# Optimization experiments

Measured on AMD Instinct MI355X. Metric: run time of the kernel, lower is better.

## Reference

```python
import jax, jax.numpy as jnp
import numpy as np

DIM = 1024
HEADS = 16

def setup_inputs() -> dict:
    key = jax.random.key(0)
    k1, k2, k3, k4 = jax.random.split(key, 4)
    x = jax.random.normal(k1, (2, 2048, DIM), dtype=jnp.float32)
    ln_gamma = jnp.ones((DIM,), dtype=jnp.float32)
    ln_beta = jnp.zeros((DIM,), dtype=jnp.float32)
    # torch Linear weight is [out, in]; store transposed [in, out] for x @ W
    W_qkv = jax.random.normal(k2, (DIM, 3 * DIM), dtype=jnp.float32) * (DIM ** -0.5)
    W_out = jax.random.normal(k3, (DIM, DIM), dtype=jnp.float32) * (DIM ** -0.5)
    b_out = jax.random.normal(k4, (DIM,), dtype=jnp.float32) * 0.02
    return {"x": x, "ln_gamma": ln_gamma, "ln_beta": ln_beta,
            "W_qkv": W_qkv, "W_out": W_out, "b_out": b_out}

def reference(x, ln_gamma, ln_beta, W_qkv, W_out, b_out):
    B, N, C = x.shape
    H = HEADS
    Dh = C // H
    scale = Dh ** -0.5
    # LayerNorm (eps=1e-5, torch default)
    mu = jnp.mean(x, axis=-1, keepdims=True)
    var = jnp.var(x, axis=-1, keepdims=True)
    xn = (x - mu) / jnp.sqrt(var + 1e-5) * ln_gamma + ln_beta
    # QKV projection: [B,N,3C] -> [3,B,H,N,Dh]
    qkv = (xn @ W_qkv).reshape(B, N, 3, H, Dh).transpose(2, 0, 3, 1, 4)
    q, k, v = qkv[0], qkv[1], qkv[2]
    attn = jnp.einsum('bhnd,bhmd->bhnm', q, k) * scale  # [B,H,N,N]
    attn = jax.nn.softmax(attn, axis=-1)
    out = jnp.einsum('bhnm,bhmd->bhnd', attn, v)  # [B,H,N,Dh]
    out = out.transpose(0, 2, 1, 3).reshape(B, N, C)
    return out @ W_out + b_out
```

## Files before the change

### kernel.cpp

```cpp
#include <hip/hip_runtime.h>
#include <hip/hip_bf16.h>

#define DIM 1024
#define HEADS 16
#define DH 64
#define SEQ 2048
#define BATCH 2
#define ROWS (BATCH*SEQ)
#define C3 (3*DIM)

typedef __attribute__((ext_vector_type(8))) short s16x8;
typedef __attribute__((ext_vector_type(4))) short s16x4;
typedef __attribute__((ext_vector_type(4))) float f32x4;
typedef __attribute__((ext_vector_type(16))) float f32x16;
typedef __attribute__((ext_vector_type(4))) unsigned int u32x4;
typedef __attribute__((ext_vector_type(2))) unsigned int u32x2;

__device__ __forceinline__ void gll16(const void* g, void* l) {
  __builtin_amdgcn_global_load_lds((const __attribute__((address_space(1))) void*)g,
                                   (__attribute__((address_space(3))) void*)l, 16, 0, 0);
}
__device__ __forceinline__ float bf2f(short s) {
  return __builtin_bit_cast(float, ((unsigned)(unsigned short)s) << 16);
}
__device__ __forceinline__ short f2bf(float f) {
  return (short)__bfloat16_as_ushort(__float2bfloat16(f));
}
__device__ __forceinline__ unsigned pk2(float a, float b) {
  unsigned lo = (unsigned)__bfloat16_as_ushort(__float2bfloat16(a));
  unsigned hh = (unsigned)__bfloat16_as_ushort(__float2bfloat16(b));
  return lo | (hh << 16);
}
__device__ __forceinline__ float fexp2(float x) {
#if __has_builtin(__builtin_amdgcn_exp2f)
  return __builtin_amdgcn_exp2f(x);
#else
  float r; asm("v_exp_f32 %0, %1" : "=v"(r) : "v"(x)); return r;
#endif
}

__global__ __launch_bounds__(256) void ln_kernel(const float* __restrict__ x,
    const float* __restrict__ gamma, const float* __restrict__ beta,
    __hip_bfloat16* __restrict__ xn) {
  int row = blockIdx.x;
  int t = threadIdx.x;
  const float4* xp = (const float4*)(x + (size_t)row * DIM);
  float4 v = xp[t];
  float s = v.x + v.y + v.z + v.w;
  float q = v.x*v.x + v.y*v.y + v.z*v.z + v.w*v.w;
  for (int off = 32; off >= 1; off >>= 1) {
    s += __shfl_xor(s, off, 64);
    q += __shfl_xor(q, off, 64);
  }
  __shared__ float red[8];
  int w = t >> 6;
  if ((t & 63) == 0) { red[w] = s; red[4 + w] = q; }
  __syncthreads();
  s = red[0] + red[1] + red[2] + red[3];
  q = red[4] + red[5] + red[6] + red[7];
  float mu = s * (1.0f / DIM);
  float var = q * (1.0f / DIM) - mu * mu;
  float rstd = rsqrtf(var + 1e-5f);
  int c = t * 4;
  float4 g4 = ((const float4*)gamma)[t];
  float4 b4 = ((const float4*)beta)[t];
  __hip_bfloat16* op = xn + (size_t)row * DIM + c;
  op[0] = __float2bfloat16((v.x - mu) * rstd * g4.x + b4.x);
  op[1] = __float2bfloat16((v.y - mu) * rstd * g4.y + b4.y);
  op[2] = __float2bfloat16((v.z - mu) * rstd * g4.z + b4.z);
  op[3] = __float2bfloat16((v.w - mu) * rstd * g4.w + b4.w);
}

__global__ __launch_bounds__(256) void transpose_cvt(const float* __restrict__ in,
    __hip_bfloat16* __restrict__ out, int R, int Cn) {
  __shared__ float tile[32][33];
  int c0 = blockIdx.x * 32, r0 = blockIdx.y * 32;
  int tx = threadIdx.x & 31, ty = threadIdx.x >> 5;
#pragma unroll
  for (int i = 0; i < 4; i++)
    tile[ty + i * 8][tx] = in[(size_t)(r0 + ty + i * 8) * Cn + c0 + tx];
  __syncthreads();
#pragma unroll
  for (int i = 0; i < 4; i++)
    out[(size_t)(c0 + ty + i * 8) * R + r0 + tx] = __float2bfloat16(tile[tx][ty + i * 8]);
}

__global__ __launch_bounds__(512) void gemm256(const __hip_bfloat16* __restrict__ A,
    const __hip_bfloat16* __restrict__ Bt, __hip_bfloat16* __restrict__ C,
    int M, int Nc, int K) {
  __shared__ short lds[2][2][256 * 64];
  const int t = threadIdx.x, l = t & 63;
  const int w = t >> 6, wr = w >> 2, wc = w & 3;
  const int m0 = blockIdx.y * 256, n0 = blockIdx.x * 256;
  const short* Ab = (const short*)A;
  const short* Bb = (const short*)Bt;
  f32x4 acc[8][4] = {};
  const int srow = t >> 3;
  const int schk = (t & 7) ^ (srow & 7);
  const int NIT = K / 64;

  {
    char* la = (char*)&lds[0][0][0];
    char* lb = (char*)&lds[0][1][0];
#pragma unroll
    for (int p = 0; p < 4; p++) {
      gll16(Ab + (size_t)(m0 + p * 64 + srow) * K + schk * 8, la + p * 8192 + t * 16);
      gll16(Bb + (size_t)(n0 + p * 64 + srow) * K + schk * 8, lb + p * 8192 + t * 16);
    }
  }
  for (int it = 0; it < NIT; ++it) {
    const int cur = it & 1;
    __syncthreads();
    if (it + 1 < NIT) {
      const int kk = (it + 1) * 64;
      char* la = (char*)&lds[cur ^ 1][0][0];
      char* lb = (char*)&lds[cur ^ 1][1][0];
#pragma unroll
      for (int p = 0; p < 4; p++) {
        gll16(Ab + (size_t)(m0 + p * 64 + srow) * K + kk + schk * 8, la + p * 8192 + t * 16);
        gll16(Bb + (size_t)(n0 + p * 64 + srow) * K + kk + schk * 8, lb + p * 8192 + t * 16);
      }
      asm volatile("s_waitcnt vmcnt(8)" ::: "memory");
    } else {
      asm volatile("s_waitcnt vmcnt(0)" ::: "memory");
    }
    __syncthreads();
    const char* la = (const char*)&lds[cur][0][0];
    const char* lb = (const char*)&lds[cur][1][0];
#pragma unroll
    for (int s = 0; s < 2; s++) {
      s16x8 af[8], bf[4];
#pragma unroll
      for (int f = 0; f < 8; f++) {
        int row = wr * 128 + f * 16 + (l & 15);
        int chk = ((s * 4 + (l >> 4)) ^ (l & 7)) * 16;
        af[f] = *(const s16x8*)(la + row * 128 + chk);
      }
#pragma unroll
      for (int n = 0; n < 4; n++) {
        int row = wc * 64 + n * 16 + (l & 15);
        int chk = ((s * 4 + (l >> 4)) ^ (l & 7)) * 16;
        bf[n] = *(const s16x8*)(lb + row * 128 + chk);
      }
#pragma unroll
      for (int f = 0; f < 8; f++)
#pragma unroll
        for (int n = 0; n < 4; n++)
          acc[f][n] = __builtin_amdgcn_mfma_f32_16x16x32_bf16(af[f], bf[n], acc[f][n], 0, 0, 0);
    }
  }
#pragma unroll
  for (int f = 0; f < 8; f++)
#pragma unroll
    for (int n = 0; n < 4; n++) {
      int col = n0 + wc * 64 + n * 16 + (l & 15);
#pragma unroll
      for (int r = 0; r < 4; r++) {
        int row = m0 + wr * 128 + f * 16 + (l >> 4) * 4 + r;
        C[(size_t)row * Nc + col] = __float2bfloat16(acc[f][n][r]);
      }
    }
}

template<int WITH_BIAS, int BN>
__global__ __launch_bounds__(256) void gemm_bt(const __hip_bfloat16* __restrict__ A,
    const __hip_bfloat16* __restrict__ Bt, void* __restrict__ Cptr,
    const float* __restrict__ bias, int M, int Nc, int K) {
  constexpr int NB = BN / 32;
  __shared__ short lds_a[128 * 32];
  __shared__ short lds_b[BN * 32];
  int t = threadIdx.x;
  int l = t & 63, w = t >> 6;
  int wr = w >> 1, wc = w & 1;
  int m0 = blockIdx.y * 128, n0 = blockIdx.x * BN;
  f32x4 acc[4][NB] = {};
  const short* Ab = (const short*)A;
  const short* Bb = (const short*)Bt;
  int srow = t >> 2;
  int scol = (t & 3) * 8;
  char* la = (char*)lds_a + (t >> 6) * 1024;
  char* lb = (char*)lds_b + (t >> 6) * 1024;
  for (int kk = 0; kk < K; kk += 32) {
    gll16(Ab + (size_t)(m0 + srow) * K + kk + scol,      la);
    gll16(Ab + (size_t)(m0 + 64 + srow) * K + kk + scol, la + 4096);
    gll16(Bb + (size_t)(n0 + srow) * K + kk + scol,      lb);
    if (BN == 128)
      gll16(Bb + (size_t)(n0 + 64 + srow) * K + kk + scol, lb + 4096);
    asm volatile("s_waitcnt vmcnt(0)" ::: "memory");
    __syncthreads();
    s16x8 af[4], bf[NB];
#pragma unroll
    for (int m = 0; m < 4; m++)
      af[m] = *(const s16x8*)&lds_a[(wr * 64 + m * 16 + (l & 15)) * 32 + (l >> 4) * 8];
#pragma unroll
    for (int n = 0; n < NB; n++)
      bf[n] = *(const s16x8*)&lds_b[(wc * (BN / 2) + n * 16 + (l & 15)) * 32 + (l >> 4) * 8];
#pragma unroll
    for (int m = 0; m < 4; m++)
#pragma unroll
      for (int n = 0; n < NB; n++)
        acc[m][n] = __builtin_amdgcn_mfma_f32_16x16x32_bf16(af[m], bf[n], acc[m][n], 0, 0, 0);
    __syncthreads();
  }
  if (WITH_BIAS) {
    float* C = (float*)Cptr;
#pragma unroll
    for (int m = 0; m < 4; m++)
#pragma unroll
      for (int n = 0; n < NB; n++) {
        int col = n0 + wc * (BN / 2) + n * 16 + (l & 15);
        float bb = bias[col];
#pragma unroll
        for (int r = 0; r < 4; r++) {
          int row = m0 + wr * 64 + m * 16 + (l >> 4) * 4 + r;
          C[(size_t)row * Nc + col] = acc[m][n][r] + bb;
        }
      }
  } else {
    __hip_bfloat16* C = (__hip_bfloat16*)Cptr;
#pragma unroll
    for (int m = 0; m < 4; m++)
#pragma unroll
      for (int n = 0; n < NB; n++) {
        int col = n0 + wc * (BN / 2) + n * 16 + (l & 15);
#pragma unroll
        for (int r = 0; r < 4; r++) {
          int row = m0 + wr * 64 + m * 16 + (l >> 4) * 4 + r;
          C[(size_t)row * Nc + col] = __float2bfloat16(acc[m][n][r]);
        }
      }
  }
}

__global__ __launch_bounds__(512) void attn_kernel(const __hip_bfloat16* __restrict__ qkv,
    __hip_bfloat16* __restrict__ attno) {
  const int t = threadIdx.x, l = t & 63, w = t >> 6;
  const int hi = l >> 5, lq = l & 31;
  const int qb = blockIdx.x, bh = blockIdx.y;
  const int b = bh >> 4, h = bh & 15;
  const short* base  = (const short*)qkv + (size_t)b * SEQ * C3 + h * DH;
  const short* kbase = base + DIM;
  const short* vbase = base + 2 * DIM;
  const int qr0 = qb * 256 + w * 32;

  __shared__ short kbuf[2][64 * 64];
  __shared__ short vbuf[2][64 * 64];

  const float SCL = 0.125f * 1.44269504089f;
  s16x8 qf[4];
#pragma unroll
  for (int dk = 0; dk < 4; dk++) {
    s16x8 raw = *(const s16x8*)(base + (size_t)(qr0 + lq) * C3 + dk * 16 + hi * 8);
#pragma unroll
    for (int j = 0; j < 8; j++) qf[dk][j] = f2bf(bf2f(raw[j]) * SCL);
  }

  s16x8 ones;
#pragma unroll
  for (int j = 0; j < 8; j++) ones[j] = (short)0x3F80;

  f32x16 o0, o1, osum;
#pragma unroll
  for (int r = 0; r < 16; r++) { o0[r] = 0.f; o1[r] = 0.f; osum[r] = 0.f; }

  const int krow = t >> 3;
  const int ksrc = (t & 7) ^ (krow & 7);
  const int vr = t & 31, vcg = t >> 5;

  {
    gll16(kbase + (size_t)krow * C3 + ksrc * 8, (char*)&kbuf[0][0] + t * 16);
    u32x2 vau = __builtin_bit_cast(u32x2, *(const s16x4*)(vbase + (size_t)(2 * vr) * C3 + vcg * 4));
    u32x2 vbu = __builtin_bit_cast(u32x2, *(const s16x4*)(vbase + (size_t)(2 * vr + 1) * C3 + vcg * 4));
    char* vd = (char*)&vbuf[0][0];
#pragma unroll
    for (int i = 0; i < 4; i++) {
      int d = vcg * 4 + i;
      unsigned dw = __builtin_amdgcn_perm(vbu[i >> 1], vau[i >> 1],
                                          (i & 1) ? 0x07060302u : 0x05040100u);
      *(unsigned*)(vd + d * 128 + (((vr >> 2) ^ (d & 7)) * 16) + (vr & 3) * 4) = dw;
    }
  }
  __syncthreads();

  for (int tile = 0; tile < SEQ / 64; ++tile) {
    const int cur = tile & 1;
    const bool pf = (tile + 1 < SEQ / 64);
    u32x2 vau, vbu;
    if (pf) {
      const int kv1 = (tile + 1) * 64;
      gll16(kbase + (size_t)(kv1 + krow) * C3 + ksrc * 8, (char*)&kbuf[cur ^ 1][0] + t * 16);
      vau = __builtin_bit_cast(u32x2, *(const s16x4*)(vbase + (size_t)(kv1 + 2 * vr) * C3 + vcg * 4));
      vbu = __builtin_bit_cast(u32x2, *(const s16x4*)(vbase + (size_t)(kv1 + 2 * vr + 1) * C3 + vcg * 4));
    }
    const char* kb = (const char*)&kbuf[cur][0];
    f32x16 st0, st1;
#pragma unroll
    for (int r = 0; r < 16; r++) { st0[r] = 0.f; st1[r] = 0.f; }
#pragma unroll
    for (int dk = 0; dk < 4; dk++) {
      int chk = ((2 * dk + hi) ^ (l & 7)) * 16;
      s16x8 kf0 = *(const s16x8*)(kb + (size_t)lq * 128 + chk);
      s16x8 kf1 = *(const s16x8*)(kb + (size_t)(32 + lq) * 128 + chk);
      st0 = __builtin_amdgcn_mfma_f32_32x32x16_bf16(kf0, qf[dk], st0, 0, 0, 0);
      st1 = __builtin_amdgcn_mfma_f32_32x32x16_bf16(kf1, qf[dk], st1, 0, 0, 0);
    }
#pragma unroll
    for (int r = 0; r < 16; r++) {
      st0[r] = fexp2(st0[r]);
      st1[r] = fexp2(st1[r]);
    }
    const char* vbp = (const char*)&vbuf[cur][0];
#pragma unroll
    for (int n = 0; n < 2; n++) {
      const f32x16& stn = n ? st1 : st0;
#pragma unroll
      for (int ksl = 0; ksl < 2; ksl++) {
        int rb = ksl * 8;
        int a  = (int)pk2(stn[rb + 0], stn[rb + 1]);
        int bq = (int)pk2(stn[rb + 2], stn[rb + 3]);
        int c  = (int)pk2(stn[rb + 4], stn[rb + 5]);
        int d  = (int)pk2(stn[rb + 6], stn[rb + 7]);
        asm volatile("v_permlane32_swap_b32 %0, %1" : "+v"(a), "+v"(c));
        asm volatile("v_permlane32_swap_b32 %0, %1" : "+v"(bq), "+v"(d));
        u32x4 fr;
        fr.x = (unsigned)a;  fr.y = (unsigned)bq;
        fr.z = (unsigned)c;  fr.w = (unsigned)d;
        s16x8 pa = __builtin_bit_cast(s16x8, fr);
        int ks = n * 2 + ksl;
        int chk = ((2 * ks + hi) ^ (l & 7)) * 16;
        s16x8 vf0 = *(const s16x8*)(vbp + (size_t)lq * 128 + chk);
        s16x8 vf1 = *(const s16x8*)(vbp + (size_t)(32 + lq) * 128 + chk);
        o0   = __builtin_amdgcn_mfma_f32_32x32x16_bf16(pa, vf0, o0, 0, 0, 0);
        o1   = __builtin_amdgcn_mfma_f32_32x32x16_bf16(pa, vf1, o1, 0, 0, 0);
        osum = __builtin_amdgcn_mfma_f32_32x32x16_bf16(pa, ones, osum, 0, 0, 0);
      }
    }
    if (pf) {
      char* vd = (char*)&vbuf[cur ^ 1][0];
#pragma unroll
      for (int i = 0; i < 4; i++) {
        int d = vcg * 4 + i;
        unsigned dw = __builtin_amdgcn_perm(vbu[i >> 1], vau[i >> 1],
                                            (i & 1) ? 0x07060302u : 0x05040100u);
        *(unsigned*)(vd + d * 128 + (((vr >> 2) ^ (d & 7)) * 16) + (vr & 3) * 4) = dw;
      }
    }
    __syncthreads();
  }
#pragma unroll
  for (int r = 0; r < 16; r++) {
    int qr = (r & 3) + 8 * (r >> 2) + 4 * hi;
    float ir = 1.0f / osum[r];
    size_t rowoff = (size_t)(b * SEQ + qr0 + qr) * DIM + h * DH;
    attno[rowoff + lq]      = __float2bfloat16(o0[r] * ir);
    attno[rowoff + 32 + lq] = __float2bfloat16(o1[r] * ir);
  }
}

extern "C" void kernel_launch(void* const* d_in, const int* in_sizes, int n_in,
                              void* d_out, int out_size, void* d_ws, size_t ws_size,
                              hipStream_t stream) {
  const float* x     = (const float*)d_in[0];
  const float* gamma = (const float*)d_in[1];
  const float* beta  = (const float*)d_in[2];
  const float* Wqkv  = (const float*)d_in[3];
  const float* Wout  = (const float*)d_in[4];
  const float* bout  = (const float*)d_in[5];

  __hip_bfloat16* xn     = (__hip_bfloat16*)d_ws;
  __hip_bfloat16* wqkv_t = xn + (size_t)ROWS * DIM;
  __hip_bfloat16* wout_t = wqkv_t + (size_t)C3 * DIM;
  __hip_bfloat16* qkv    = wout_t + (size_t)DIM * DIM;
  __hip_bfloat16* attno  = qkv + (size_t)ROWS * C3;

  ln_kernel<<<ROWS, 256, 0, stream>>>(x, gamma, beta, xn);
  transpose_cvt<<<dim3(C3 / 32, DIM / 32), 256, 0, stream>>>(Wqkv, wqkv_t, DIM, C3);
  transpose_cvt<<<dim3(DIM / 32, DIM / 32), 256, 0, stream>>>(Wout, wout_t, DIM, DIM);
  gemm256<<<dim3(C3 / 256, ROWS / 256), 512, 0, stream>>>(xn, wqkv_t, qkv, ROWS, C3, DIM);
  attn_kernel<<<dim3(SEQ / 256, BATCH * HEADS), 512, 0, stream>>>(qkv, attno);
  gemm_bt<1, 64><<<dim3(DIM / 64, ROWS / 128), 256, 0, stream>>>(attno, wout_t, d_out, bout, ROWS, DIM, DIM);
}
```

Baseline: 130.2 us.

## Double-buffer out-projection GEMM and load attention K directly into registers

```diff
diff --git a/kernel.cpp b/kernel.cpp
--- a/kernel.cpp
+++ b/kernel.cpp
@@ -8,6 +8,7 @@
 #define BATCH 2
 #define ROWS (BATCH*SEQ)
 #define C3 (3*DIM)
+#define NT (SEQ/64)
 
 typedef __attribute__((ext_vector_type(8))) short s16x8;
 typedef __attribute__((ext_vector_type(4))) short s16x4;
@@ -162,74 +163,66 @@
     }
 }
 
-template<int WITH_BIAS, int BN>
-__global__ __launch_bounds__(256) void gemm_bt(const __hip_bfloat16* __restrict__ A,
-    const __hip_bfloat16* __restrict__ Bt, void* __restrict__ Cptr,
-    const float* __restrict__ bias, int M, int Nc, int K) {
-  constexpr int NB = BN / 32;
-  __shared__ short lds_a[128 * 32];
-  __shared__ short lds_b[BN * 32];
-  int t = threadIdx.x;
-  int l = t & 63, w = t >> 6;
-  int wr = w >> 1, wc = w & 1;
-  int m0 = blockIdx.y * 128, n0 = blockIdx.x * BN;
-  f32x4 acc[4][NB] = {};
+__global__ __launch_bounds__(256) void gemm_out(const __hip_bfloat16* __restrict__ A,
+    const __hip_bfloat16* __restrict__ Bt, float* __restrict__ C,
+    const float* __restrict__ bias) {
+  __shared__ short lds_a[2][128 * 32];
+  __shared__ short lds_b[2][64 * 32];
+  const int t = threadIdx.x, l = t & 63, w = t >> 6;
+  const int wr = w >> 1, wc = w & 1;
+  const int m0 = blockIdx.y * 128, n0 = blockIdx.x * 64;
   const short* Ab = (const short*)A;
   const short* Bb = (const short*)Bt;
-  int srow = t >> 2;
-  int scol = (t & 3) * 8;
-  char* la = (char*)lds_a + (t >> 6) * 1024;
-  char* lb = (char*)lds_b + (t >> 6) * 1024;
-  for (int kk = 0; kk < K; kk += 32) {
-    gll16(Ab + (size_t)(m0 + srow) * K + kk + scol,      la);
-    gll16(Ab + (size_t)(m0 + 64 + srow) * K + kk + scol, la + 4096);
-    gll16(Bb + (size_t)(n0 + srow) * K + kk + scol,      lb);
-    if (BN == 128)
-      gll16(Bb + (size_t)(n0 + 64 + srow) * K + kk + scol, lb + 4096);
-    asm volatile("s_waitcnt vmcnt(0)" ::: "memory");
+  const int K = DIM;
+  f32x4 acc[4][2] = {};
+  const int srow = t >> 2, scol = (t & 3) * 8;
+  {
+    char* la = (char*)&lds_a[0][0];
+    char* lb = (char*)&lds_b[0][0];
+    gll16(Ab + (size_t)(m0 + srow) * K + scol,      la + t * 16);
+    gll16(Ab + (size_t)(m0 + 64 + srow) * K + scol, la + 4096 + t * 16);
+    gll16(Bb + (size_t)(n0 + srow) * K + scol,      lb + t * 16);
+  }
+  for (int it = 0; it < K / 32; ++it) {
+    const int cur = it & 1;
     __syncthreads();
-    s16x8 af[4], bf[NB];
+    if (it + 1 < K / 32) {
+      const int kk = (it + 1) * 32;
+      char* la = (char*)&lds_a[cur ^ 1][0];
+      char* lb = (char*)&lds_b[cur ^ 1][0];
+      gll16(Ab + (size_t)(m0 + srow) * K + kk + scol,      la + t * 16);
+      gll16(Ab + (size_t)(m0 + 64 + srow) * K + kk + scol, la + 4096 + t * 16);
+      gll16(Bb + (size_t)(n0 + srow) * K + kk + scol,      lb + t * 16);
+      asm volatile("s_waitcnt vmcnt(3)" ::: "memory");
+    } else {
+      asm volatile("s_waitcnt vmcnt(0)" ::: "memory");
+    }
+    __syncthreads();
+    s16x8 af[4], bf[2];
 #pragma unroll
     for (int m = 0; m < 4; m++)
-      af[m] = *(const s16x8*)&lds_a[(wr * 64 + m * 16 + (l & 15)) * 32 + (l >> 4) * 8];
-#pragma unroll
-    for (int n = 0; n < NB; n++)
-      bf[n] = *(const s16x8*)&lds_b[(wc * (BN / 2) + n * 16 + (l & 15)) * 32 + (l >> 4) * 8];
+      af[m] = *(const s16x8*)&lds_a[cur][(wr * 64 + m * 16 + (l & 15)) * 32 + (l >> 4) * 8];
+#pragma unroll
+    for (int n = 0; n < 2; n++)
+      bf[n] = *(const s16x8*)&lds_b[cur][(wc * 32 + n * 16 + (l & 15)) * 32 + (l >> 4) * 8];
 #pragma unroll
     for (int m = 0; m < 4; m++)
 #pragma unroll
-      for (int n = 0; n < NB; n++)
+      for (int n = 0; n < 2; n++)
         acc[m][n] = __builtin_amdgcn_mfma_f32_16x16x32_bf16(af[m], bf[n], acc[m][n], 0, 0, 0);
-    __syncthreads();
-  }
-  if (WITH_BIAS) {
-    float* C = (float*)Cptr;
-#pragma unroll
-    for (int m = 0; m < 4; m++)
-#pragma unroll
-      for (int n = 0; n < NB; n++) {
-        int col = n0 + wc * (BN / 2) + n * 16 + (l & 15);
-        float bb = bias[col];
-#pragma unroll
-        for (int r = 0; r < 4; r++) {
-          int row = m0 + wr * 64 + m * 16 + (l >> 4) * 4 + r;
-          C[(size_t)row * Nc + col] = acc[m][n][r] + bb;
-        }
-      }
-  } else {
-    __hip_bfloat16* C = (__hip_bfloat16*)Cptr;
-#pragma unroll
-    for (int m = 0; m < 4; m++)
-#pragma unroll
-      for (int n = 0; n < NB; n++) {
-        int col = n0 + wc * (BN / 2) + n * 16 + (l & 15);
-#pragma unroll
-        for (int r = 0; r < 4; r++) {
-          int row = m0 + wr * 64 + m * 16 + (l >> 4) * 4 + r;
-          C[(size_t)row * Nc + col] = __float2bfloat16(acc[m][n][r]);
-        }
-      }
-  }
+  }
+#pragma unroll
+  for (int m = 0; m < 4; m++)
+#pragma unroll
+    for (int n = 0; n < 2; n++) {
+      int col = n0 + wc * 32 + n * 16 + (l & 15);
+      float bb = bias[col];
+#pragma unroll
+      for (int r = 0; r < 4; r++) {
+        int row = m0 + wr * 64 + m * 16 + (l >> 4) * 4 + r;
+        C[(size_t)row * DIM + col] = acc[m][n][r] + bb;
+      }
+    }
 }
 
 __global__ __launch_bounds__(512) void attn_kernel(const __hip_bfloat16* __restrict__ qkv,
@@ -243,7 +236,6 @@
   const short* vbase = base + 2 * DIM;
   const int qr0 = qb * 256 + w * 32;
 
-  __shared__ short kbuf[2][64 * 64];
   __shared__ short vbuf[2][64 * 64];
 
   const float SCL = 0.125f * 1.44269504089f;
@@ -263,12 +255,18 @@
 #pragma unroll
   for (int r = 0; r < 16; r++) { o0[r] = 0.f; o1[r] = 0.f; osum[r] = 0.f; }
 
-  const int krow = t >> 3;
-  const int ksrc = (t & 7) ^ (krow & 7);
   const int vr = t & 31, vcg = t >> 5;
-
+  const short* kp0 = kbase + (size_t)lq * C3 + hi * 8;
+  const short* kp1 = kbase + (size_t)(32 + lq) * C3 + hi * 8;
+
+  s16x8 ka0[4], ka1[4], kb0[4], kb1[4];
+
+#pragma unroll
+  for (int dk = 0; dk < 4; dk++) {
+    ka0[dk] = *(const s16x8*)(kp0 + dk * 16);
+    ka1[dk] = *(const s16x8*)(kp1 + dk * 16);
+  }
   {
-    gll16(kbase + (size_t)krow * C3 + ksrc * 8, (char*)&kbuf[0][0] + t * 16);
     u32x2 vau = __builtin_bit_cast(u32x2, *(const s16x4*)(vbase + (size_t)(2 * vr) * C3 + vcg * 4));
     u32x2 vbu = __builtin_bit_cast(u32x2, *(const s16x4*)(vbase + (size_t)(2 * vr + 1) * C3 + vcg * 4));
     char* vd = (char*)&vbuf[0][0];
@@ -282,71 +280,82 @@
   }
   __syncthreads();
 
-  for (int tile = 0; tile < SEQ / 64; ++tile) {
-    const int cur = tile & 1;
-    const bool pf = (tile + 1 < SEQ / 64);
-    u32x2 vau, vbu;
-    if (pf) {
-      const int kv1 = (tile + 1) * 64;
-      gll16(kbase + (size_t)(kv1 + krow) * C3 + ksrc * 8, (char*)&kbuf[cur ^ 1][0] + t * 16);
-      vau = __builtin_bit_cast(u32x2, *(const s16x4*)(vbase + (size_t)(kv1 + 2 * vr) * C3 + vcg * 4));
-      vbu = __builtin_bit_cast(u32x2, *(const s16x4*)(vbase + (size_t)(kv1 + 2 * vr + 1) * C3 + vcg * 4));
-    }
-    const char* kb = (const char*)&kbuf[cur][0];
-    f32x16 st0, st1;
-#pragma unroll
-    for (int r = 0; r < 16; r++) { st0[r] = 0.f; st1[r] = 0.f; }
-#pragma unroll
-    for (int dk = 0; dk < 4; dk++) {
-      int chk = ((2 * dk + hi) ^ (l & 7)) * 16;
-      s16x8 kf0 = *(const s16x8*)(kb + (size_t)lq * 128 + chk);
-      s16x8 kf1 = *(const s16x8*)(kb + (size_t)(32 + lq) * 128 + chk);
-      st0 = __builtin_amdgcn_mfma_f32_32x32x16_bf16(kf0, qf[dk], st0, 0, 0, 0);
-      st1 = __builtin_amdgcn_mfma_f32_32x32x16_bf16(kf1, qf[dk], st1, 0, 0, 0);
-    }
-#pragma unroll
-    for (int r = 0; r < 16; r++) {
-      st0[r] = fexp2(st0[r]);
-      st1[r] = fexp2(st1[r]);
-    }
-    const char* vbp = (const char*)&vbuf[cur][0];
-#pragma unroll
-    for (int n = 0; n < 2; n++) {
-      const f32x16& stn = n ? st1 : st0;
-#pragma unroll
-      for (int ksl = 0; ksl < 2; ksl++) {
-        int rb = ksl * 8;
-        int a  = (int)pk2(stn[rb + 0], stn[rb + 1]);
-        int bq = (int)pk2(stn[rb + 2], stn[rb + 3]);
-        int c  = (int)pk2(stn[rb + 4], stn[rb + 5]);
-        int d  = (int)pk2(stn[rb + 6], stn[rb + 7]);
-        asm volatile("v_permlane32_swap_b32 %0, %1" : "+v"(a), "+v"(c));
-        asm volatile("v_permlane32_swap_b32 %0, %1" : "+v"(bq), "+v"(d));
-        u32x4 fr;
-        fr.x = (unsigned)a;  fr.y = (unsigned)bq;
-        fr.z = (unsigned)c;  fr.w = (unsigned)d;
-        s16x8 pa = __builtin_bit_cast(s16x8, fr);
-        int ks = n * 2 + ksl;
-        int chk = ((2 * ks + hi) ^ (l & 7)) * 16;
-        s16x8 vf0 = *(const s16x8*)(vbp + (size_t)lq * 128 + chk);
-        s16x8 vf1 = *(const s16x8*)(vbp + (size_t)(32 + lq) * 128 + chk);
-        o0   = __builtin_amdgcn_mfma_f32_32x32x16_bf16(pa, vf0, o0, 0, 0, 0);
-        o1   = __builtin_amdgcn_mfma_f32_32x32x16_bf16(pa, vf1, o1, 0, 0, 0);
-        osum = __builtin_amdgcn_mfma_f32_32x32x16_bf16(pa, ones, osum, 0, 0, 0);
-      }
-    }
-    if (pf) {
-      char* vd = (char*)&vbuf[cur ^ 1][0];
-#pragma unroll
-      for (int i = 0; i < 4; i++) {
-        int d = vcg * 4 + i;
-        unsigned dw = __builtin_amdgcn_perm(vbu[i >> 1], vau[i >> 1],
-                                            (i & 1) ? 0x07060302u : 0x05040100u);
-        *(unsigned*)(vd + d * 128 + (((vr >> 2) ^ (d & 7)) * 16) + (vr & 3) * 4) = dw;
-      }
-    }
-    __syncthreads();
-  }
+#define ATTN_BODY(TILE, VCUR, VNXT, KC0, KC1, KN0, KN1)                         \
+  {                                                                             \
+    const int tile_ = (TILE);                                                   \
+    const bool pf_ = (tile_ + 1 < NT);                                          \
+    u32x2 vau_, vbu_;                                                           \
+    if (pf_) {                                                                  \
+      const size_t koff_ = (size_t)(tile_ + 1) * 64 * C3;                       \
+      _Pragma("unroll")                                                         \
+      for (int dk = 0; dk < 4; dk++) {                                          \
+        KN0[dk] = *(const s16x8*)(kp0 + koff_ + dk * 16);                       \
+        KN1[dk] = *(const s16x8*)(kp1 + koff_ + dk * 16);                       \
+      }                                                                         \
+      const int kv1_ = (tile_ + 1) * 64;                                        \
+      vau_ = __builtin_bit_cast(u32x2,                                          \
+          *(const s16x4*)(vbase + (size_t)(kv1_ + 2 * vr) * C3 + vcg * 4));     \
+      vbu_ = __builtin_bit_cast(u32x2,                                          \
+          *(const s16x4*)(vbase + (size_t)(kv1_ + 2 * vr + 1) * C3 + vcg * 4)); \
+    }                                                                           \
+    f32x16 st0, st1;                                                            \
+    _Pragma("unroll")                                                           \
+    for (int r = 0; r < 16; r++) { st0[r] = 0.f; st1[r] = 0.f; }                \
+    _Pragma("unroll")                                                           \
+    for (int dk = 0; dk < 4; dk++) {                                            \
+      st0 = __builtin_amdgcn_mfma_f32_32x32x16_bf16(KC0[dk], qf[dk], st0, 0, 0, 0); \
+      st1 = __builtin_amdgcn_mfma_f32_32x32x16_bf16(KC1[dk], qf[dk], st1, 0, 0, 0); \
+    }                                                                           \
+    _Pragma("unroll")                                                           \
+    for (int r = 0; r < 16; r++) {                                              \
+      st0[r] = fexp2(st0[r]);                                                   \
+      st1[r] = fexp2(st1[r]);                                                   \
+    }                                                                           \
+    const char* vbp_ = (const char*)&VCUR[0];                                   \
+    _Pragma("unroll")                                                           \
+    for (int n = 0; n < 2; n++) {                                               \
+      const f32x16& stn = n ? st1 : st0;                                        \
+      _Pragma("unroll")                                                         \
+      for (int ksl = 0; ksl < 2; ksl++) {                                       \
+        int rb = ksl * 8;                                                       \
+        int a_  = (int)pk2(stn[rb + 0], stn[rb + 1]);                           \
+        int b_  = (int)pk2(stn[rb + 2], stn[rb + 3]);                           \
+        int c_  = (int)pk2(stn[rb + 4], stn[rb + 5]);                           \
+        int d_  = (int)pk2(stn[rb + 6], stn[rb + 7]);                           \
+        asm volatile("v_permlane32_swap_b32 %0, %1" : "+v"(a_), "+v"(c_));      \
+        asm volatile("v_permlane32_swap_b32 %0, %1" : "+v"(b_), "+v"(d_));      \
+        u32x4 fr;                                                               \
+        fr.x = (unsigned)a_;  fr.y = (unsigned)b_;                              \
+        fr.z = (unsigned)c_;  fr.w = (unsigned)d_;                              \
+        s16x8 pa = __builtin_bit_cast(s16x8, fr);                               \
+        int ks = n * 2 + ksl;                                                   \
+        int chk = ((2 * ks + hi) ^ (l & 7)) * 16;                               \
+        s16x8 vf0 = *(const s16x8*)(vbp_ + (size_t)lq * 128 + chk);             \
+        s16x8 vf1 = *(const s16x8*)(vbp_ + (size_t)(32 + lq) * 128 + chk);      \
+        o0   = __builtin_amdgcn_mfma_f32_32x32x16_bf16(pa, vf0, o0, 0, 0, 0);   \
+        o1   = __builtin_amdgcn_mfma_f32_32x32x16_bf16(pa, vf1, o1, 0, 0, 0);   \
+        osum = __builtin_amdgcn_mfma_f32_32x32x16_bf16(pa, ones, osum, 0, 0, 0);\
+      }                                                                         \
+    }                                                                           \
+    if (pf_) {                                                                  \
+      char* vd_ = (char*)&VNXT[0];                                              \
+      _Pragma("unroll")                                                         \
+      for (int i = 0; i < 4; i++) {                                             \
+        int d = vcg * 4 + i;                                                    \
+        unsigned dw = __builtin_amdgcn_perm(vbu_[i >> 1], vau_[i >> 1],         \
+                                            (i & 1) ? 0x07060302u : 0x05040100u); \
+        *(unsigned*)(vd_ + d * 128 + (((vr >> 2) ^ (d & 7)) * 16) + (vr & 3) * 4) = dw; \
+      }                                                                         \
+    }                                                                           \
+    __syncthreads();                                                            \
+  }
+
+  for (int t2 = 0; t2 < NT / 2; ++t2) {
+    ATTN_BODY(2 * t2,     vbuf[0], vbuf[1], ka0, ka1, kb0, kb1)
+    ATTN_BODY(2 * t2 + 1, vbuf[1], vbuf[0], kb0, kb1, ka0, ka1)
+  }
+#undef ATTN_BODY
+
 #pragma unroll
   for (int r = 0; r < 16; r++) {
     int qr = (r & 3) + 8 * (r >> 2) + 4 * hi;
@@ -378,5 +387,5 @@
   transpose_cvt<<<dim3(DIM / 32, DIM / 32), 256, 0, stream>>>(Wout, wout_t, DIM, DIM);
   gemm256<<<dim3(C3 / 256, ROWS / 256), 512, 0, stream>>>(xn, wqkv_t, qkv, ROWS, C3, DIM);
   attn_kernel<<<dim3(SEQ / 256, BATCH * HEADS), 512, 0, stream>>>(qkv, attno);
-  gemm_bt<1, 64><<<dim3(DIM / 64, ROWS / 128), 256, 0, stream>>>(attno, wout_t, d_out, bout, ROWS, DIM, DIM);
-}
+  gemm_out<<<dim3(DIM / 64, ROWS / 128), 256, 0, stream>>>(attno, wout_t, (float*)d_out, bout);
+}
```

After: 175.3 us. +34.7%, slower.
